# Performance work log

Hardware: AMD Instinct MI355X
Metric: run time of the kernel (lower is better)

## Reference

```python
import jax, jax.numpy as jnp
import numpy as np

# Static config (matches init_kwargs / input_specs)
B, CIN, H, W = 8, 32, 96, 96
OC, KH, KW = 64, 3, 3
SH, SW = 1, 1
PAD = 1
P = 3                      # num_points
POS_MIN, POS_MAX = -1.0, 1.0
OH = (H + 2 * PAD - KH) // SH + 1   # 96
OW = (W + 2 * PAD - KW) // SW + 1   # 96
K = CIN * KH * KW                    # 288 reduction elements
S = OH * OW                          # 9216 output positions


def setup_inputs() -> dict:
    key = jax.random.key(0)
    k1, k2, k3 = jax.random.split(key, 3)
    x = jax.random.normal(k1, (B, CIN, H, W), dtype=jnp.float32)
    # positions: shared linspace over position_range, expanded per weight
    pos = jnp.broadcast_to(
        jnp.linspace(POS_MIN, POS_MAX, P, dtype=jnp.float32),
        (OC, CIN, KH, KW, P),
    )
    # values: linear ramp between two small random endpoints (start, end)
    start = 0.01 * jax.random.normal(k2, (OC, CIN, KH, KW), dtype=jnp.float32)
    end = 0.01 * jax.random.normal(k3, (OC, CIN, KH, KW), dtype=jnp.float32)
    w = jnp.linspace(0.0, 1.0, P, dtype=jnp.float32)
    values = start[..., None] * (1.0 - w) + end[..., None] * w
    return {"x": x, "positions": pos, "values": values}


def _unfold(x):
    """F.unfold equivalent: [B,CIN,H,W] -> [B, CIN*KH*KW, OH*OW], (c,kh,kw) order."""
    xp = jnp.pad(x, ((0, 0), (0, 0), (PAD, PAD), (PAD, PAD)))
    cols = [
        xp[:, :, kh : kh + OH * SH : SH, kw : kw + OW * SW : SW]
        for kh in range(KH)
        for kw in range(KW)
    ]
    patches = jnp.stack(cols, axis=2)  # [B, CIN, KH*KW, OH, OW]
    return patches.reshape(B, K, S)


def _piecewise_conv(x, positions, values):
    patches = _unfold(x)                      # [B, K, S]
    pos = positions.reshape(OC, K, P)
    val = values.reshape(OC, K, P)
    dp = pos[..., 1:] - pos[..., :-1]         # [OC, K, P-1]
    dv = val[..., 1:] - val[..., :-1]
    # slope 0 on degenerate intervals (pos_i == pos_{i+1} contributes val_i, as in kernel)
    slopes = jnp.where(dp > 0, dv / jnp.where(dp > 0, dp, 1.0), 0.0)

    # f(x) = val_0 + sum_i slope_i * (clip(x, pos_i, pos_{i+1}) - pos_i)
    # Exactly reproduces the kernel's piecewise-linear interp with left/right clamping
    # for sorted positions. Scan over the K reduction axis keeps the [B,OC,S]
    # broadcast intermediate small.
    xs = (
        patches.transpose(1, 0, 2),   # [K, B, S]
        pos.transpose(1, 0, 2),       # [K, OC, P]
        val.transpose(1, 0, 2),       # [K, OC, P]
        slopes.transpose(1, 0, 2),    # [K, OC, P-1]
    )

    def step(acc, inp):
        xk, pk, vk, sk = inp          # [B,S], [OC,P], [OC,P], [OC,P-1]
        f = jnp.broadcast_to(vk[None, :, 0, None], (B, OC, S))
        for i in range(P - 1):        # P is small & static
            t = jnp.clip(xk[:, None, :], pk[None, :, i, None], pk[None, :, i + 1, None])
            f = f + sk[None, :, i, None] * (t - pk[None, :, i, None])
        return acc + f, None

    out, _ = jax.lax.scan(step, jnp.zeros((B, OC, S), x.dtype), xs)
    return out.reshape(B, OC, OH, OW)


def reference(x, positions, values):
    return _piecewise_conv(x, positions, values)
```

## Files before the change

### kernel.cpp

```cpp
#include <hip/hip_runtime.h>


typedef _Float16 half8 __attribute__((ext_vector_type(8)));
typedef float floatx4 __attribute__((ext_vector_type(4)));
typedef float floatx16 __attribute__((ext_vector_type(16)));

#define CIN   32
#define OCN   64
#define HW    96
#define NCOL  98
#define NSTEP 36
#define WS_A_HALVES (NSTEP * 2 * 64 * 8)

__global__ __launch_bounds__(128) void prep_kernel(
    const float* __restrict__ pos, const float* __restrict__ val,
    _Float16* __restrict__ wsA, float* __restrict__ bias) {
  const int oc = blockIdx.x;
  const int t = threadIdx.x;
  __shared__ float csum[128];
  float cacc = 0.f;
  const float p0 = pos[0], p1 = pos[1], p2 = pos[2];
  const float r01 = (p1 > p0) ? 1.f / (p1 - p0) : 0.f;
  const float r12 = (p2 > p1) ? 1.f / (p2 - p1) : 0.f;
  if (t < 72) {
    const int s = t >> 1, khalf = t & 1;
    const int kk = s >> 1, s2 = s & 1;
    const int khkw = kk >> 1, c2 = kk & 1;
    half8 h;
#pragma unroll
    for (int j = 0; j < 8; ++j) {
      const int cin = s2 * 16 + khalf * 8 + j;
      const float* vb = val + ((size_t)(oc * CIN + cin) * 9 + khkw) * 3;
      const float V0 = vb[0], V1 = vb[1], V2 = vb[2];
      const float s0 = (V1 - V0) * r01, s1 = (V2 - V1) * r12;
      h[j] = (_Float16)(c2 ? s1 : s0);
      if (c2 == 0) cacc += V0 - s0 * p0 - s1 * p1;
    }
    *reinterpret_cast<half8*>(
        &wsA[(((size_t)s * 2 + (oc >> 5)) * 64 + khalf * 32 + (oc & 31)) * 8]) = h;
  }
  csum[t] = cacc;
  __syncthreads();
  for (int st = 64; st > 0; st >>= 1) {
    if (t < st) csum[t] += csum[t + st];
    __syncthreads();
  }
  if (t == 0) bias[oc] = csum[0];
}

__global__ __launch_bounds__(384, 5) void pwconv_kernel(
    const float* __restrict__ x, const float* __restrict__ pos,
    const _Float16* __restrict__ wsA, const float* __restrict__ bias,
    float* __restrict__ out) {
  const int blk = blockIdx.x;
  const int b  = blk & 7;
  const int oh = blk >> 3;
  const int tid = threadIdx.x;

  __shared__ alignas(16) _Float16 Bs[2 * 3 * 4 * NCOL * 8];

  const float p0 = pos[0], p1 = pos[1], p2 = pos[2];

  const int lane = tid & 63;
  const int wv   = tid >> 6;
  const int mG   = wv >> 1 == 0 ? 0 : (wv >= 3 ? 1 : 0);
  const int mG2  = wv / 3;
  const int nf   = wv % 3;
  const int l31  = lane & 31;
  const int q2   = lane >> 5;
  (void)mG;

  const _Float16* abase = wsA + (size_t)lane * 8;
  half8 a_cur = *reinterpret_cast<const half8*>(abase + (size_t)(0 * 2 + mG2) * 64 * 8);

  if (tid < 288) {
    const int cg  = tid % 24;
    const int t2  = tid / 24;
    const int chi = t2 & 3;
    const int row = t2 >> 2;
    const int xr = oh + row - 1;
    floatx4 v[8];
    if (xr >= 0 && xr < HW) {
      const float* src = x + (((size_t)b * CIN + chi * 8) * HW + xr) * HW + cg * 4;
#pragma unroll
      for (int j = 0; j < 8; ++j)
        v[j] = *reinterpret_cast<const floatx4*>(src + (size_t)j * HW * HW);
    } else {
#pragma unroll
      for (int j = 0; j < 8; ++j) v[j] = (floatx4){0.f, 0.f, 0.f, 0.f};
    }
#pragma unroll
    for (int c = 0; c < 4; ++c) {
      half8 a0, a1;
#pragma unroll
      for (int j = 0; j < 8; ++j) {
        const float tv = v[j][c];
        a0[j] = (_Float16)fminf(fmaxf(tv, p0), p1);
        a1[j] = (_Float16)fminf(fmaxf(tv, p1), p2);
      }
      const int col = 1 + cg * 4 + c;
      *reinterpret_cast<half8*>(&Bs[(((0 * 3 + row) * 4 + chi) * NCOL + col) * 8]) = a0;
      *reinterpret_cast<half8*>(&Bs[(((1 * 3 + row) * 4 + chi) * NCOL + col) * 8]) = a1;
    }
  } else if (tid < 312) {
    const int ht = tid - 288;
    const int col = (ht & 1) ? 97 : 0;
    const int chi = (ht >> 1) & 3;
    const int row = ht >> 3;
    const _Float16 h0 = (_Float16)fminf(fmaxf(0.f, p0), p1);
    const _Float16 h1 = (_Float16)fminf(fmaxf(0.f, p1), p2);
    half8 a0, a1;
#pragma unroll
    for (int j = 0; j < 8; ++j) { a0[j] = h0; a1[j] = h1; }
    *reinterpret_cast<half8*>(&Bs[(((0 * 3 + row) * 4 + chi) * NCOL + col) * 8]) = a0;
    *reinterpret_cast<half8*>(&Bs[(((1 * 3 + row) * 4 + chi) * NCOL + col) * 8]) = a1;
  }
  __syncthreads();

  floatx16 acc;
#pragma unroll
  for (int i = 0; i < 16; ++i) acc[i] = 0.f;

  const int lbase = q2 * NCOL + nf * 32 + l31;

#pragma unroll
  for (int s = 0; s < NSTEP; ++s) {
    half8 a_nxt;
    if (s + 1 < NSTEP)
      a_nxt = *reinterpret_cast<const half8*>(
          abase + (size_t)((s + 1) * 2 + mG2) * 64 * 8);
    const int khkw = s >> 2;
    const int c2   = (s >> 1) & 1;
    const int s2   = s & 1;
    const int kh   = khkw / 3;
    const int kw   = khkw - kh * 3;
    const half8 bf = *reinterpret_cast<const half8*>(
        &Bs[(((c2 * 3 + kh) * 4 + s2 * 2) * NCOL + kw + lbase) * 8]);
    acc = __builtin_amdgcn_mfma_f32_32x32x16_f16(a_cur, bf, acc, 0, 0, 0);
    a_cur = a_nxt;
  }

  const int ow = nf * 32 + l31;
#pragma unroll
  for (int g = 0; g < 4; ++g) {
    const int ocb = mG2 * 32 + g * 8 + q2 * 4;
    const floatx4 bv = *reinterpret_cast<const floatx4*>(&bias[ocb]);
#pragma unroll
    for (int i = 0; i < 4; ++i) {
      const size_t idx = (((size_t)b * OCN + ocb + i) * HW + oh) * HW + ow;
      out[idx] = acc[g * 4 + i] + bv[i];
    }
  }
}

extern "C" void kernel_launch(void* const* d_in, const int* in_sizes, int n_in,
                              void* d_out, int out_size, void* d_ws, size_t ws_size,
                              hipStream_t stream) {
  const float* x   = (const float*)d_in[0];
  const float* pos = (const float*)d_in[1];
  const float* val = (const float*)d_in[2];
  _Float16* wsA = (_Float16*)d_ws;
  float* bias = (float*)((char*)d_ws + WS_A_HALVES * 2);
  float* outp = (float*)d_out;

  prep_kernel<<<64, 128, 0, stream>>>(pos, val, wsA, bias);
  pwconv_kernel<<<8 * HW, 384, 0, stream>>>(x, pos, wsA, bias, outp);
}
```

Baseline: 80.16 us.

## Compute two output rows per block with 2x2 MFMA register tiling

Each block now computes two output rows with 3 waves instead of one row with 6 waves. Each wave holds four accumulators covering both OC halves and both rows, so every A fragment and B fragment load feeds two MFMAs. The shared-memory input tile grows to 4 halo rows, shared across the two output rows, which cuts redundant global loads of x and halo conversion. The cost is more registers per thread, fewer blocks (384), and a deeper A prefetch.

```diff
diff --git a/kernel.cpp b/kernel.cpp
--- a/kernel.cpp
+++ b/kernel.cpp
@@ -48,37 +48,41 @@
   if (t == 0) bias[oc] = csum[0];
 }
 
-__global__ __launch_bounds__(384, 5) void pwconv_kernel(
+__global__ __launch_bounds__(192, 3) void pwconv_kernel(
     const float* __restrict__ x, const float* __restrict__ pos,
     const _Float16* __restrict__ wsA, const float* __restrict__ bias,
     float* __restrict__ out) {
   const int blk = blockIdx.x;
-  const int b  = blk & 7;
-  const int oh = blk >> 3;
+  const int b   = blk & 7;
+  const int ohp = blk >> 3;
+  const int oh0 = ohp * 2;
   const int tid = threadIdx.x;
 
-  __shared__ alignas(16) _Float16 Bs[2 * 3 * 4 * NCOL * 8];
+  __shared__ alignas(16) _Float16 Bs[2 * 4 * 4 * NCOL * 8];
 
   const float p0 = pos[0], p1 = pos[1], p2 = pos[2];
 
   const int lane = tid & 63;
-  const int wv   = tid >> 6;
-  const int mG   = wv >> 1 == 0 ? 0 : (wv >= 3 ? 1 : 0);
-  const int mG2  = wv / 3;
-  const int nf   = wv % 3;
+  const int nf   = tid >> 6;
   const int l31  = lane & 31;
   const int q2   = lane >> 5;
-  (void)mG;
 
   const _Float16* abase = wsA + (size_t)lane * 8;
-  half8 a_cur = *reinterpret_cast<const half8*>(abase + (size_t)(0 * 2 + mG2) * 64 * 8);
+  half8 a0p[2], a1p[2];
+#pragma unroll
+  for (int s = 0; s < 2; ++s) {
+    a0p[s] = *reinterpret_cast<const half8*>(abase + (size_t)(s * 2 + 0) * 512);
+    a1p[s] = *reinterpret_cast<const half8*>(abase + (size_t)(s * 2 + 1) * 512);
+  }
 
-  if (tid < 288) {
-    const int cg  = tid % 24;
-    const int t2  = tid / 24;
+#pragma unroll
+  for (int it = 0; it < 2; ++it) {
+    const int item = tid + it * 192;
+    const int cg  = item % 24;
+    const int t2  = item / 24;
     const int chi = t2 & 3;
     const int row = t2 >> 2;
-    const int xr = oh + row - 1;
+    const int xr  = oh0 + row - 1;
     floatx4 v[8];
     if (xr >= 0 && xr < HW) {
       const float* src = x + (((size_t)b * CIN + chi * 8) * HW + xr) * HW + cg * 4;
@@ -91,66 +95,85 @@
     }
 #pragma unroll
     for (int c = 0; c < 4; ++c) {
-      half8 a0, a1;
+      half8 h0, h1;
 #pragma unroll
       for (int j = 0; j < 8; ++j) {
         const float tv = v[j][c];
-        a0[j] = (_Float16)fminf(fmaxf(tv, p0), p1);
-        a1[j] = (_Float16)fminf(fmaxf(tv, p1), p2);
+        h0[j] = (_Float16)fminf(fmaxf(tv, p0), p1);
+        h1[j] = (_Float16)fminf(fmaxf(tv, p1), p2);
       }
       const int col = 1 + cg * 4 + c;
-      *reinterpret_cast<half8*>(&Bs[(((0 * 3 + row) * 4 + chi) * NCOL + col) * 8]) = a0;
-      *reinterpret_cast<half8*>(&Bs[(((1 * 3 + row) * 4 + chi) * NCOL + col) * 8]) = a1;
+      *reinterpret_cast<half8*>(&Bs[(((0 * 4 + row) * 4 + chi) * NCOL + col) * 8]) = h0;
+      *reinterpret_cast<half8*>(&Bs[(((1 * 4 + row) * 4 + chi) * NCOL + col) * 8]) = h1;
     }
-  } else if (tid < 312) {
-    const int ht = tid - 288;
-    const int col = (ht & 1) ? 97 : 0;
-    const int chi = (ht >> 1) & 3;
-    const int row = ht >> 3;
+  }
+  if (tid < 32) {
+    const int side = tid & 1;
+    const int chi  = (tid >> 1) & 3;
+    const int row  = tid >> 3;
+    const int col  = side ? 97 : 0;
     const _Float16 h0 = (_Float16)fminf(fmaxf(0.f, p0), p1);
     const _Float16 h1 = (_Float16)fminf(fmaxf(0.f, p1), p2);
     half8 a0, a1;
 #pragma unroll
     for (int j = 0; j < 8; ++j) { a0[j] = h0; a1[j] = h1; }
-    *reinterpret_cast<half8*>(&Bs[(((0 * 3 + row) * 4 + chi) * NCOL + col) * 8]) = a0;
-    *reinterpret_cast<half8*>(&Bs[(((1 * 3 + row) * 4 + chi) * NCOL + col) * 8]) = a1;
+    *reinterpret_cast<half8*>(&Bs[(((0 * 4 + row) * 4 + chi) * NCOL + col) * 8]) = a0;
+    *reinterpret_cast<half8*>(&Bs[(((1 * 4 + row) * 4 + chi) * NCOL + col) * 8]) = a1;
   }
   __syncthreads();
 
-  floatx16 acc;
+  floatx16 acc00, acc01, acc10, acc11;
 #pragma unroll
-  for (int i = 0; i < 16; ++i) acc[i] = 0.f;
+  for (int i = 0; i < 16; ++i) {
+    acc00[i] = 0.f; acc01[i] = 0.f; acc10[i] = 0.f; acc11[i] = 0.f;
+  }
 
   const int lbase = q2 * NCOL + nf * 32 + l31;
 
 #pragma unroll
   for (int s = 0; s < NSTEP; ++s) {
-    half8 a_nxt;
-    if (s + 1 < NSTEP)
-      a_nxt = *reinterpret_cast<const half8*>(
-          abase + (size_t)((s + 1) * 2 + mG2) * 64 * 8);
+    const int sl = s & 1;
+    const half8 a0 = a0p[sl];
+    const half8 a1 = a1p[sl];
+    if (s + 2 < NSTEP) {
+      a0p[sl] = *reinterpret_cast<const half8*>(abase + (size_t)((s + 2) * 2 + 0) * 512);
+      a1p[sl] = *reinterpret_cast<const half8*>(abase + (size_t)((s + 2) * 2 + 1) * 512);
+    }
     const int khkw = s >> 2;
     const int c2   = (s >> 1) & 1;
     const int s2   = s & 1;
     const int kh   = khkw / 3;
     const int kw   = khkw - kh * 3;
-    const half8 bf = *reinterpret_cast<const half8*>(
-        &Bs[(((c2 * 3 + kh) * 4 + s2 * 2) * NCOL + kw + lbase) * 8]);
-    acc = __builtin_amdgcn_mfma_f32_32x32x16_f16(a_cur, bf, acc, 0, 0, 0);
-    a_cur = a_nxt;
+    const half8 bf0 = *reinterpret_cast<const half8*>(
+        &Bs[(((c2 * 4 + kh + 0) * 4 + s2 * 2) * NCOL + kw + lbase) * 8]);
+    const half8 bf1 = *reinterpret_cast<const half8*>(
+        &Bs[(((c2 * 4 + kh + 1) * 4 + s2 * 2) * NCOL + kw + lbase) * 8]);
+    acc00 = __builtin_amdgcn_mfma_f32_32x32x16_f16(a0, bf0, acc00, 0, 0, 0);
+    acc10 = __builtin_amdgcn_mfma_f32_32x32x16_f16(a1, bf0, acc10, 0, 0, 0);
+    acc01 = __builtin_amdgcn_mfma_f32_32x32x16_f16(a0, bf1, acc01, 0, 0, 0);
+    acc11 = __builtin_amdgcn_mfma_f32_32x32x16_f16(a1, bf1, acc11, 0, 0, 0);
   }
 
   const int ow = nf * 32 + l31;
-#pragma unroll
-  for (int g = 0; g < 4; ++g) {
-    const int ocb = mG2 * 32 + g * 8 + q2 * 4;
-    const floatx4 bv = *reinterpret_cast<const floatx4*>(&bias[ocb]);
-#pragma unroll
-    for (int i = 0; i < 4; ++i) {
-      const size_t idx = (((size_t)b * OCN + ocb + i) * HW + oh) * HW + ow;
-      out[idx] = acc[g * 4 + i] + bv[i];
-    }
+#define STORE_TILE(ACC, MI, NI)                                                \
+  {                                                                            \
+    const int oh = oh0 + (NI);                                                 \
+    _Pragma("unroll")                                                          \
+    for (int g = 0; g < 4; ++g) {                                              \
+      const int ocb = (MI) * 32 + g * 8 + q2 * 4;                              \
+      const floatx4 bv = *reinterpret_cast<const floatx4*>(&bias[ocb]);        \
+      _Pragma("unroll")                                                        \
+      for (int i = 0; i < 4; ++i) {                                            \
+        const size_t idx = (((size_t)b * OCN + ocb + i) * HW + oh) * HW + ow;  \
+        out[idx] = (ACC)[g * 4 + i] + bv[i];                                   \
+      }                                                                        \
+    }                                                                          \
   }
+  STORE_TILE(acc00, 0, 0)
+  STORE_TILE(acc10, 1, 0)
+  STORE_TILE(acc01, 0, 1)
+  STORE_TILE(acc11, 1, 1)
+#undef STORE_TILE
 }
 
 extern "C" void kernel_launch(void* const* d_in, const int* in_sizes, int n_in,
@@ -164,5 +187,5 @@
   float* outp = (float*)d_out;
 
   prep_kernel<<<64, 128, 0, stream>>>(pos, val, wsA, bias);
-  pwconv_kernel<<<8 * HW, 384, 0, stream>>>(x, pos, wsA, bias, outp);
+  pwconv_kernel<<<8 * (HW / 2), 192, 0, stream>>>(x, pos, wsA, bias, outp);
 }
```

New measurement: 84.20 us. 1.05x slower.
